# Kernel tuning notes

Measured on AMD Instinct MI355X. Metric: run time of the kernel, lower is better.

Reference implementation:

```python
import jax, jax.numpy as jnp
import numpy as np

B, F, NP, DIM, H, DH = 4, 16, 196, 512, 8, 64  # batch, frames, patches, dim, heads, dim_head
N = 1 + F * NP  # sequence length incl CLS


def setup_inputs() -> dict:
    key = jax.random.key(0)
    k1, k2, k3, k4 = jax.random.split(key, 4)
    return {
        "x": jax.random.normal(k1, (B, N, DIM), dtype=jnp.float32),
        "W_qkv": jax.random.normal(k2, (DIM, 3 * H * DH), dtype=jnp.float32) * 0.05,
        "W_out": jax.random.normal(k3, (H * DH, DIM), dtype=jnp.float32) * 0.05,
        "b_out": jax.random.normal(k4, (DIM,), dtype=jnp.float32) * 0.05,
        "f": F,
    }


def _attn(q, k, v):
    # q: [bb, i, d], k/v: [bb, j, d]
    sim = jnp.einsum('bid,bjd->bij', q, k)
    a = jax.nn.softmax(sim, axis=-1)
    return jnp.einsum('bij,bjd->bid', a, v)


def reference(x, W_qkv, W_out, b_out, f):
    b, n_tot, dim = x.shape
    h, d = H, DH
    scale = d ** (-0.5)
    qkv = x @ W_qkv  # [b, N, 3*h*d]
    q, k, v = jnp.split(qkv, 3, axis=-1)

    def to_bh(t):  # b n (h d) -> (b h) n d
        return t.reshape(b, n_tot, h, d).transpose(0, 2, 1, 3).reshape(b * h, n_tot, d)

    q, k, v = map(to_bh, (q, k, v))
    q = q * scale

    cls_q, q_ = q[:, :1], q[:, 1:]
    cls_k, k_ = k[:, :1], k[:, 1:]
    cls_v, v_ = v[:, :1], v[:, 1:]

    # CLS token attends over the full sequence
    cls_out = _attn(cls_q, k, v)  # [(b h), 1, d]

    # spatial factorization: (b h) (f n) d -> (b h f) n d
    n = (n_tot - 1) // f
    def split_f(t):
        return t.reshape(b * h * f, n, d)
    q_, k_, v_ = map(split_f, (q_, k_, v_))

    # repeat CLS k/v per frame: b () d -> (b r) () d with r = f
    cls_k_r = jnp.repeat(cls_k, f, axis=0)
    cls_v_r = jnp.repeat(cls_v, f, axis=0)
    k_ = jnp.concatenate([cls_k_r, k_], axis=1)  # [(b h f), n+1, d]
    v_ = jnp.concatenate([cls_v_r, v_], axis=1)

    out = _attn(q_, k_, v_)  # [(b h f), n, d]
    out = out.reshape(b * h, f * n, d)
    out = jnp.concatenate([cls_out, out], axis=1)  # [(b h), N, d]
    out = out.reshape(b, h, n_tot, d).transpose(0, 2, 1, 3).reshape(b, n_tot, h * d)
    return out @ W_out + b_out
```

## Files before the change

kernel.cpp:

```cpp
#include <hip/hip_runtime.h>
#include <math.h>

#define B_   4
#define F_   16
#define NP_  196
#define DIM_ 512
#define H_   8
#define DH_  64
#define NTOT 3137
#define BH_  32
#define MROWS 12548
#define QSZ_ ((size_t)BH_ * NTOT * DH_)
#define KVPAD 224
#define PSTRIDE 232
#define NCHUNK 13

typedef unsigned short u16;
typedef __attribute__((ext_vector_type(8))) short    bf16x8;
typedef __attribute__((ext_vector_type(8))) unsigned short u16x8;
typedef __attribute__((ext_vector_type(4))) unsigned short u16x4;
typedef __attribute__((ext_vector_type(4))) float    f32x4;

__device__ __forceinline__ u16 f2bf(float f) {
    unsigned int u = __float_as_uint(f);
    unsigned int r = (u + 0x7FFFu + ((u >> 16) & 1u)) >> 16;
    return (u16)r;
}
__device__ __forceinline__ float bf2f(u16 u) {
    return __uint_as_float(((unsigned int)u) << 16);
}

__device__ __forceinline__ void gl2lds16(const u16* g, u16* l) {
    __builtin_amdgcn_global_load_lds(
        (const __attribute__((address_space(1))) unsigned int*)(g),
        (__attribute__((address_space(3))) unsigned int*)(l),
        16, 0, 0);
}

__global__ __launch_bounds__(256) void convert_x_kernel(
    const float* __restrict__ x, u16* __restrict__ xbf)
{
    int idx = blockIdx.x * 256 + threadIdx.x;
    float4 v = ((const float4*)x)[idx];
    u16x4 p = { f2bf(v.x), f2bf(v.y), f2bf(v.z), f2bf(v.w) };
    *(u16x4*)(&xbf[(size_t)idx * 4]) = p;
}

__global__ __launch_bounds__(256) void transpose_bf16_kernel(
    const float* __restrict__ src, u16* __restrict__ dst, int R, int C)
{
    __shared__ float t[32][33];
    const int tx = threadIdx.x & 31, ty = threadIdx.x >> 5;
    const int c0 = blockIdx.x * 32, r0 = blockIdx.y * 32;
    #pragma unroll
    for (int i = 0; i < 4; ++i) {
        int r = ty + i * 8;
        t[r][tx] = src[(size_t)(r0 + r) * C + c0 + tx];
    }
    __syncthreads();
    #pragma unroll
    for (int i = 0; i < 4; ++i) {
        int cc = ty + i * 8;
        dst[(size_t)(c0 + cc) * R + r0 + tx] = f2bf(t[tx][cc]);
    }
}

template<int MODE, int MI>
__global__ __launch_bounds__(256, 2) void gemm_bf16_mfma(
    const u16* __restrict__ A, const u16* __restrict__ BT,
    u16* __restrict__ Cq, u16* __restrict__ Ck, u16* __restrict__ Cv,
    float* __restrict__ Cout, const float* __restrict__ bias)
{
    constexpr int ASUB = MI * 2;
    __shared__ alignas(16) u16 Asm[2][ASUB * 512];
    __shared__ alignas(16) u16 Bsm[2][8 * 512];

    const int tid  = threadIdx.x;
    const int wave = tid >> 6, lane = tid & 63;
    const int wr = wave >> 1, wc = wave & 1;
    const int lm = lane & 15, lq = lane >> 4;
    const int row0 = blockIdx.y * (MI * 32);
    const int col0 = blockIdx.x * 128;

    f32x4 acc[MI][4];
    #pragma unroll
    for (int i = 0; i < MI; ++i)
        #pragma unroll
        for (int j = 0; j < 4; ++j) acc[i][j] = (f32x4){0.f, 0.f, 0.f, 0.f};

    auto stage = [&](int k0, int buf) {
        #pragma unroll
        for (int i = 0; i < ASUB / 4; ++i) {
            int s = wave * (ASUB / 4) + i;
            int arow = row0 + s * 16 + lm;
            if (arow >= MROWS) arow = MROWS - 1;
            gl2lds16(A + (size_t)arow * 512 + k0 + lq * 8, &Asm[buf][s * 512 + lane * 8]);
        }
        #pragma unroll
        for (int i = 0; i < 2; ++i) {
            int s = wave * 2 + i;
            int brow = col0 + s * 16 + lm;
            gl2lds16(BT + (size_t)brow * 512 + k0 + lq * 8, &Bsm[buf][s * 512 + lane * 8]);
        }
    };

    stage(0, 0);
    for (int it = 0; it < 16; ++it) {
        __syncthreads();
        if (it < 15) stage((it + 1) * 32, (it + 1) & 1);
        const int buf = it & 1;
        bf16x8 af[MI], bf[4];
        #pragma unroll
        for (int mi = 0; mi < MI; ++mi)
            af[mi] = *(const bf16x8*)(&Asm[buf][(wr * MI + mi) * 512 + lane * 8]);
        #pragma unroll
        for (int ni = 0; ni < 4; ++ni)
            bf[ni] = *(const bf16x8*)(&Bsm[buf][(wc * 4 + ni) * 512 + lane * 8]);
        #pragma unroll
        for (int mi = 0; mi < MI; ++mi)
            #pragma unroll
            for (int ni = 0; ni < 4; ++ni)
                acc[mi][ni] = __builtin_amdgcn_mfma_f32_16x16x32_bf16(
                    af[mi], bf[ni], acc[mi][ni], 0, 0, 0);
    }

    if (MODE == 0) {
        const int t3 = col0 >> 9;
        #pragma unroll
        for (int mi = 0; mi < MI; ++mi) {
            #pragma unroll
            for (int r = 0; r < 4; ++r) {
                int gr = row0 + wr * (MI * 16) + mi * 16 + lq * 4 + r;
                if (gr >= MROWS) continue;
                int b = gr / NTOT;
                int n = gr - b * NTOT;
                #pragma unroll
                for (int ni = 0; ni < 4; ++ni) {
                    int gc = col0 + wc * 64 + ni * 16 + lm;
                    int rem = gc & 511;
                    int h = rem >> 6, d = rem & 63;
                    size_t tok = (size_t)(b * H_ + h) * NTOT + n;
                    float v = acc[mi][ni][r];
                    if (t3 == 0)      Cq[tok * 64 + d] = f2bf(v * 0.125f);
                    else if (t3 == 1) Ck[tok * 64 + d] = f2bf(v);
                    else              Cv[tok * 64 + d] = f2bf(v);
                }
            }
        }
    } else {
        float bb[4];
        #pragma unroll
        for (int ni = 0; ni < 4; ++ni)
            bb[ni] = bias[col0 + wc * 64 + ni * 16 + lm];
        #pragma unroll
        for (int mi = 0; mi < MI; ++mi) {
            #pragma unroll
            for (int r = 0; r < 4; ++r) {
                int gr = row0 + wr * (MI * 16) + mi * 16 + lq * 4 + r;
                if (gr >= MROWS) continue;
                #pragma unroll
                for (int ni = 0; ni < 4; ++ni) {
                    int gc = col0 + wc * 64 + ni * 16 + lm;
                    Cout[(size_t)gr * 512 + gc] = acc[mi][ni][r] + bb[ni];
                }
            }
        }
    }
}

__global__ __launch_bounds__(256) void vt_build_kernel(
    const u16* __restrict__ vb, u16* __restrict__ vT)
{
    const int g = blockIdx.x;
    const int bh = g >> 4, f = g & 15;
    const int d = threadIdx.x & 63, jq = threadIdx.x >> 6;
    const int j0 = blockIdx.y * 32;
    u16* dst = vT + ((size_t)g * 64 + d) * KVPAD;
    #pragma unroll
    for (int i = 0; i < 8; ++i) {
        int jj = j0 + i * 4 + jq;
        u16 val = 0;
        if (jj <= 196) {
            int n = (jj == 0) ? 0 : (1 + f * NP_ + jj - 1);
            val = vb[((size_t)bh * NTOT + n) * 64 + d];
        }
        dst[jj] = val;
    }
}

__global__ __launch_bounds__(256) void attn_mfma_kernel(
    const u16* __restrict__ qb, const u16* __restrict__ kb,
    const u16* __restrict__ vT, u16* __restrict__ attn)
{
    __shared__ alignas(16) u16 Pbuf[4 * 16 * PSTRIDE];

    const int tid  = threadIdx.x;
    const int wave = tid >> 6, lane = tid & 63;
    const int lm = lane & 15, lq = lane >> 4;
    const int task = blockIdx.x * 4 + wave;
    const int mt = task % 13;
    const int gf = task / 13;
    const int f  = gf & 15;
    const int bh = gf >> 4;

    const int rq = min(mt * 16 + lm, 195);
    const u16* qrow = qb + ((size_t)bh * NTOT + (1 + f * NP_ + rq)) * 64;
    bf16x8 qf0 = *(const bf16x8*)(qrow + lq * 8);
    bf16x8 qf1 = *(const bf16x8*)(qrow + 32 + lq * 8);

    f32x4 S[13];
    #pragma unroll
    for (int nt = 0; nt < 13; ++nt) {
        int rkc = min(nt * 16 + lm, 196);
        int nk = (rkc == 0) ? 0 : (1 + f * NP_ + rkc - 1);
        const u16* krow = kb + ((size_t)bh * NTOT + nk) * 64;
        bf16x8 kf0 = *(const bf16x8*)(krow + lq * 8);
        bf16x8 kf1 = *(const bf16x8*)(krow + 32 + lq * 8);
        f32x4 z = (f32x4){0.f, 0.f, 0.f, 0.f};
        z = __builtin_amdgcn_mfma_f32_16x16x32_bf16(qf0, kf0, z, 0, 0, 0);
        z = __builtin_amdgcn_mfma_f32_16x16x32_bf16(qf1, kf1, z, 0, 0, 0);
        S[nt] = z;
    }

    #pragma unroll
    for (int nt = 0; nt < 13; ++nt)
        if (nt * 16 + lm >= 197) {
            S[nt][0] = -INFINITY; S[nt][1] = -INFINITY;
            S[nt][2] = -INFINITY; S[nt][3] = -INFINITY;
        }

    float invl[4];
    #pragma unroll
    for (int r = 0; r < 4; ++r) {
        float mx = -INFINITY;
        #pragma unroll
        for (int nt = 0; nt < 13; ++nt) mx = fmaxf(mx, S[nt][r]);
        mx = fmaxf(mx, __shfl_xor(mx, 1, 64));
        mx = fmaxf(mx, __shfl_xor(mx, 2, 64));
        mx = fmaxf(mx, __shfl_xor(mx, 4, 64));
        mx = fmaxf(mx, __shfl_xor(mx, 8, 64));
        float sum = 0.f;
        #pragma unroll
        for (int nt = 0; nt < 13; ++nt) {
            float p = __expf(S[nt][r] - mx);
            S[nt][r] = p;
            sum += p;
        }
        sum += __shfl_xor(sum, 1, 64);
        sum += __shfl_xor(sum, 2, 64);
        sum += __shfl_xor(sum, 4, 64);
        sum += __shfl_xor(sum, 8, 64);
        invl[r] = 1.f / sum;
    }

    u16* P = Pbuf + wave * 16 * PSTRIDE;
    #pragma unroll
    for (int nt = 0; nt < 13; ++nt) {
        int col = nt * 16 + lm;
        #pragma unroll
        for (int r = 0; r < 4; ++r)
            P[(lq * 4 + r) * PSTRIDE + col] = f2bf(S[nt][r]);
    }
    {
        u16x4 z4 = {0, 0, 0, 0};
        *(u16x4*)(P + lm * PSTRIDE + 208 + lq * 4) = z4;
    }

    f32x4 O[4];
    #pragma unroll
    for (int nd = 0; nd < 4; ++nd) O[nd] = (f32x4){0.f, 0.f, 0.f, 0.f};
    const u16* vbase = vT + (size_t)(bh * 16 + f) * 64 * KVPAD;
    #pragma unroll
    for (int ks = 0; ks < 7; ++ks) {
        bf16x8 pf = *(const bf16x8*)(P + lm * PSTRIDE + ks * 32 + lq * 8);
        #pragma unroll
        for (int nd = 0; nd < 4; ++nd) {
            bf16x8 vf = *(const bf16x8*)(vbase + (size_t)(nd * 16 + lm) * KVPAD + ks * 32 + lq * 8);
            O[nd] = __builtin_amdgcn_mfma_f32_16x16x32_bf16(pf, vf, O[nd], 0, 0, 0);
        }
    }

    const int b = bh >> 3, h = bh & 7;
    #pragma unroll
    for (int r = 0; r < 4; ++r) {
        int rql = mt * 16 + lq * 4 + r;
        if (rql >= 196) continue;
        int n = 1 + f * NP_ + rql;
        u16* dst = attn + ((size_t)b * NTOT + n) * 512 + h * 64;
        float s = invl[r];
        #pragma unroll
        for (int nd = 0; nd < 4; ++nd)
            dst[nd * 16 + lm] = f2bf(O[nd][r] * s);
    }
}

__global__ __launch_bounds__(256) void attn_cls_partial_kernel(
    const u16* __restrict__ qb, const u16* __restrict__ kb,
    const u16* __restrict__ vb, float* __restrict__ cls_m,
    float* __restrict__ cls_l, float* __restrict__ cls_o)
{
    __shared__ float qs[64];
    __shared__ float redm[4], redl[4];
    __shared__ float ps[256];
    __shared__ float so[4][64];

    const int c = blockIdx.x, bh = blockIdx.y;
    const int t = threadIdx.x;
    const int lane = t & 63, w = t >> 6;

    if (t < 64) qs[t] = bf2f(qb[(size_t)bh * NTOT * 64 + t]);
    __syncthreads();

    const int j = c * 256 + t;
    const bool valid = (j < NTOT);
    const int jc = valid ? j : (NTOT - 1);
    const u16* krow = kb + ((size_t)bh * NTOT + jc) * 64;
    float s0 = 0.f, s1 = 0.f, s2 = 0.f, s3 = 0.f;
    #pragma unroll
    for (int i = 0; i < 8; ++i) {
        u16x8 k8 = *(const u16x8*)(krow + i * 8);
        const float* qp = qs + i * 8;
        s0 = fmaf(qp[0], bf2f(k8[0]), s0);
        s1 = fmaf(qp[1], bf2f(k8[1]), s1);
        s2 = fmaf(qp[2], bf2f(k8[2]), s2);
        s3 = fmaf(qp[3], bf2f(k8[3]), s3);
        s0 = fmaf(qp[4], bf2f(k8[4]), s0);
        s1 = fmaf(qp[5], bf2f(k8[5]), s1);
        s2 = fmaf(qp[6], bf2f(k8[6]), s2);
        s3 = fmaf(qp[7], bf2f(k8[7]), s3);
    }
    float s = (s0 + s1) + (s2 + s3);
    if (!valid) s = -INFINITY;

    float mx = s;
    #pragma unroll
    for (int off = 1; off < 64; off <<= 1) mx = fmaxf(mx, __shfl_xor(mx, off, 64));
    if (lane == 0) redm[w] = mx;
    __syncthreads();
    mx = fmaxf(fmaxf(redm[0], redm[1]), fmaxf(redm[2], redm[3]));

    float pv = __expf(s - mx);
    float l = pv;
    #pragma unroll
    for (int off = 1; off < 64; off <<= 1) l += __shfl_xor(l, off, 64);
    if (lane == 0) redl[w] = l;
    ps[t] = pv;
    __syncthreads();
    l = redl[0] + redl[1] + redl[2] + redl[3];

    const int d = lane, part = w;
    float o = 0.f;
    #pragma unroll 8
    for (int i = 0; i < 64; ++i) {
        int jj = c * 256 + part * 64 + i;
        int jjc = (jj < NTOT) ? jj : (NTOT - 1);
        o = fmaf(ps[part * 64 + i], bf2f(vb[((size_t)bh * NTOT + jjc) * 64 + d]), o);
    }
    so[part][d] = o;
    __syncthreads();
    if (t < 64) {
        float O = so[0][t] + so[1][t] + so[2][t] + so[3][t];
        int pi = bh * NCHUNK + c;
        cls_o[(size_t)pi * 64 + t] = O;
        if (t == 0) { cls_m[pi] = mx; cls_l[pi] = l; }
    }
}

__global__ __launch_bounds__(64) void attn_cls_merge_kernel(
    const float* __restrict__ cls_m, const float* __restrict__ cls_l,
    const float* __restrict__ cls_o, u16* __restrict__ attn)
{
    const int bh = blockIdx.x, lane = threadIdx.x;
    float M = -INFINITY;
    #pragma unroll
    for (int p = 0; p < NCHUNK; ++p) M = fmaxf(M, cls_m[bh * NCHUNK + p]);
    float L = 0.f, O = 0.f;
    #pragma unroll
    for (int p = 0; p < NCHUNK; ++p) {
        float al = __expf(cls_m[bh * NCHUNK + p] - M);
        L += cls_l[bh * NCHUNK + p] * al;
        O += cls_o[(size_t)(bh * NCHUNK + p) * 64 + lane] * al;
    }
    const int b = bh >> 3, h = bh & 7;
    attn[(size_t)b * NTOT * 512 + h * 64 + lane] = f2bf(O / L);
}

extern "C" void kernel_launch(void* const* d_in, const int* in_sizes, int n_in,
                              void* d_out, int out_size, void* d_ws, size_t ws_size,
                              hipStream_t stream) {
    const float* x    = (const float*)d_in[0];
    const float* wqkv = (const float*)d_in[1];
    const float* wout = (const float*)d_in[2];
    const float* bout = (const float*)d_in[3];

    u16* p = (u16*)d_ws;
    u16* xbf   = p;                    p += (size_t)MROWS * 512;
    u16* attn  = xbf;
    u16* wqkvT = p;                    p += (size_t)1536 * 512;
    u16* woutT = p;                    p += (size_t)512 * 512;
    u16* qbuf  = p;                    p += QSZ_;
    u16* kbuf  = p;                    p += QSZ_;
    u16* vbuf  = p;                    p += QSZ_;
    u16* vT    = p;                    p += (size_t)BH_ * 16 * 64 * KVPAD;
    float* clsws = (float*)p;
    float* cls_m = clsws;
    float* cls_l = clsws + BH_ * NCHUNK;
    float* cls_o = clsws + 2 * BH_ * NCHUNK;
    float* outp  = (float*)d_out;

    convert_x_kernel<<<6274, 256, 0, stream>>>(x, xbf);
    transpose_bf16_kernel<<<dim3(48, 16), 256, 0, stream>>>(wqkv, wqkvT, 512, 1536);
    transpose_bf16_kernel<<<dim3(16, 16), 256, 0, stream>>>(wout, woutT, 512, 512);
    gemm_bf16_mfma<0, 8><<<dim3(12, 50), 256, 0, stream>>>(
        xbf, wqkvT, qbuf, kbuf, vbuf, nullptr, nullptr);
    vt_build_kernel<<<dim3(512, 7), 256, 0, stream>>>(vbuf, vT);
    attn_mfma_kernel<<<1664, 256, 0, stream>>>(qbuf, kbuf, vT, attn);
    attn_cls_partial_kernel<<<dim3(NCHUNK, 32), 256, 0, stream>>>(
        qbuf, kbuf, vbuf, cls_m, cls_l, cls_o);
    attn_cls_merge_kernel<<<32, 64, 0, stream>>>(cls_m, cls_l, cls_o, attn);
    gemm_bf16_mfma<1, 4><<<dim3(4, 99), 256, 0, stream>>>(
        attn, woutT, nullptr, nullptr, nullptr, outp, bout);
}
```

Measured before the change: 268.7 us.

## Restructure GEMM to keep full-K B tile in LDS and stream A from global

The bf16 MFMA GEMM now loads the entire 64-column by 512-K slice of the transposed weight into LDS once per block, then has each wave read its A rows directly from global memory into registers, with no per-K-step staging or barriers. The old version double-buffered both A and B in LDS. Tiles become 256 rows by 64 columns, so the grids change, and the QKV epilogue hoists the head, destination buffer and scale out of the inner loop. This removes the LDS round-trip and the synchronisation for A. In exchange, A loads are uncoalesced-ish direct global reads, B uses 64KB of LDS, and occupancy may drop.

```diff
diff --git a/kernel.cpp b/kernel.cpp
--- a/kernel.cpp
+++ b/kernel.cpp
@@ -65,104 +65,93 @@
     }
 }
 
-template<int MODE, int MI>
-__global__ __launch_bounds__(256, 2) void gemm_bf16_mfma(
+template<int MODE>
+__global__ __launch_bounds__(256) void gemm_bf16_mfma(
     const u16* __restrict__ A, const u16* __restrict__ BT,
     u16* __restrict__ Cq, u16* __restrict__ Ck, u16* __restrict__ Cv,
     float* __restrict__ Cout, const float* __restrict__ bias)
 {
-    constexpr int ASUB = MI * 2;
-    __shared__ alignas(16) u16 Asm[2][ASUB * 512];
-    __shared__ alignas(16) u16 Bsm[2][8 * 512];
+    __shared__ alignas(16) u16 Bs[64 * 512];
 
     const int tid  = threadIdx.x;
     const int wave = tid >> 6, lane = tid & 63;
-    const int wr = wave >> 1, wc = wave & 1;
     const int lm = lane & 15, lq = lane >> 4;
-    const int row0 = blockIdx.y * (MI * 32);
-    const int col0 = blockIdx.x * 128;
-
-    f32x4 acc[MI][4];
-    #pragma unroll
-    for (int i = 0; i < MI; ++i)
+    const int col0 = blockIdx.x * 64;
+    const int rows0 = blockIdx.y * 256;
+
+    #pragma unroll
+    for (int i = 0; i < 16; ++i) {
+        int sub = wave * 16 + i;
+        int s = sub >> 2, n = sub & 3;
+        gl2lds16(BT + (size_t)(col0 + n * 16 + lm) * 512 + s * 32 + lq * 8,
+                 &Bs[sub * 512 + lane * 8]);
+    }
+    __syncthreads();
+
+    const int rbase = rows0 + wave * 64;
+    const u16* aptr[4];
+    #pragma unroll
+    for (int ri = 0; ri < 4; ++ri) {
+        int r = rbase + ri * 16 + lm;
+        if (r >= MROWS) r = MROWS - 1;
+        aptr[ri] = A + (size_t)r * 512 + lq * 8;
+    }
+
+    f32x4 acc[4][4];
+    #pragma unroll
+    for (int i = 0; i < 4; ++i)
         #pragma unroll
         for (int j = 0; j < 4; ++j) acc[i][j] = (f32x4){0.f, 0.f, 0.f, 0.f};
 
-    auto stage = [&](int k0, int buf) {
-        #pragma unroll
-        for (int i = 0; i < ASUB / 4; ++i) {
-            int s = wave * (ASUB / 4) + i;
-            int arow = row0 + s * 16 + lm;
-            if (arow >= MROWS) arow = MROWS - 1;
-            gl2lds16(A + (size_t)arow * 512 + k0 + lq * 8, &Asm[buf][s * 512 + lane * 8]);
-        }
-        #pragma unroll
-        for (int i = 0; i < 2; ++i) {
-            int s = wave * 2 + i;
-            int brow = col0 + s * 16 + lm;
-            gl2lds16(BT + (size_t)brow * 512 + k0 + lq * 8, &Bsm[buf][s * 512 + lane * 8]);
-        }
-    };
-
-    stage(0, 0);
-    for (int it = 0; it < 16; ++it) {
-        __syncthreads();
-        if (it < 15) stage((it + 1) * 32, (it + 1) & 1);
-        const int buf = it & 1;
-        bf16x8 af[MI], bf[4];
-        #pragma unroll
-        for (int mi = 0; mi < MI; ++mi)
-            af[mi] = *(const bf16x8*)(&Asm[buf][(wr * MI + mi) * 512 + lane * 8]);
+    #pragma unroll 4
+    for (int s = 0; s < 16; ++s) {
+        bf16x8 bfr[4];
         #pragma unroll
         for (int ni = 0; ni < 4; ++ni)
-            bf[ni] = *(const bf16x8*)(&Bsm[buf][(wc * 4 + ni) * 512 + lane * 8]);
-        #pragma unroll
-        for (int mi = 0; mi < MI; ++mi)
+            bfr[ni] = *(const bf16x8*)(&Bs[(s * 4 + ni) * 512 + lane * 8]);
+        #pragma unroll
+        for (int ri = 0; ri < 4; ++ri) {
+            bf16x8 af = *(const bf16x8*)(aptr[ri] + s * 32);
             #pragma unroll
             for (int ni = 0; ni < 4; ++ni)
-                acc[mi][ni] = __builtin_amdgcn_mfma_f32_16x16x32_bf16(
-                    af[mi], bf[ni], acc[mi][ni], 0, 0, 0);
+                acc[ri][ni] = __builtin_amdgcn_mfma_f32_16x16x32_bf16(
+                    af, bfr[ni], acc[ri][ni], 0, 0, 0);
+        }
     }
 
     if (MODE == 0) {
         const int t3 = col0 >> 9;
-        #pragma unroll
-        for (int mi = 0; mi < MI; ++mi) {
+        const int h  = (col0 >> 6) & 7;
+        u16* dst3 = (t3 == 0) ? Cq : (t3 == 1) ? Ck : Cv;
+        const float scale = (t3 == 0) ? 0.125f : 1.0f;
+        #pragma unroll
+        for (int ri = 0; ri < 4; ++ri) {
             #pragma unroll
             for (int r = 0; r < 4; ++r) {
-                int gr = row0 + wr * (MI * 16) + mi * 16 + lq * 4 + r;
+                int gr = rbase + ri * 16 + lq * 4 + r;
                 if (gr >= MROWS) continue;
                 int b = gr / NTOT;
                 int n = gr - b * NTOT;
+                size_t tok = (size_t)(b * H_ + h) * NTOT + n;
                 #pragma unroll
-                for (int ni = 0; ni < 4; ++ni) {
-                    int gc = col0 + wc * 64 + ni * 16 + lm;
-                    int rem = gc & 511;
-                    int h = rem >> 6, d = rem & 63;
-                    size_t tok = (size_t)(b * H_ + h) * NTOT + n;
-                    float v = acc[mi][ni][r];
-                    if (t3 == 0)      Cq[tok * 64 + d] = f2bf(v * 0.125f);
-                    else if (t3 == 1) Ck[tok * 64 + d] = f2bf(v);
-                    else              Cv[tok * 64 + d] = f2bf(v);
-                }
+                for (int ni = 0; ni < 4; ++ni)
+                    dst3[tok * 64 + ni * 16 + lm] = f2bf(acc[ri][ni][r] * scale);
             }
         }
     } else {
         float bb[4];
         #pragma unroll
         for (int ni = 0; ni < 4; ++ni)
-            bb[ni] = bias[col0 + wc * 64 + ni * 16 + lm];
-        #pragma unroll
-        for (int mi = 0; mi < MI; ++mi) {
+            bb[ni] = bias[col0 + ni * 16 + lm];
+        #pragma unroll
+        for (int ri = 0; ri < 4; ++ri) {
             #pragma unroll
             for (int r = 0; r < 4; ++r) {
-                int gr = row0 + wr * (MI * 16) + mi * 16 + lq * 4 + r;
+                int gr = rbase + ri * 16 + lq * 4 + r;
                 if (gr >= MROWS) continue;
                 #pragma unroll
-                for (int ni = 0; ni < 4; ++ni) {
-                    int gc = col0 + wc * 64 + ni * 16 + lm;
-                    Cout[(size_t)gr * 512 + gc] = acc[mi][ni][r] + bb[ni];
-                }
+                for (int ni = 0; ni < 4; ++ni)
+                    Cout[(size_t)gr * 512 + col0 + ni * 16 + lm] = acc[ri][ni][r] + bb[ni];
             }
         }
     }
@@ -411,13 +400,13 @@
     convert_x_kernel<<<6274, 256, 0, stream>>>(x, xbf);
     transpose_bf16_kernel<<<dim3(48, 16), 256, 0, stream>>>(wqkv, wqkvT, 512, 1536);
     transpose_bf16_kernel<<<dim3(16, 16), 256, 0, stream>>>(wout, woutT, 512, 512);
-    gemm_bf16_mfma<0, 8><<<dim3(12, 50), 256, 0, stream>>>(
+    gemm_bf16_mfma<0><<<dim3(24, 50), 256, 0, stream>>>(
         xbf, wqkvT, qbuf, kbuf, vbuf, nullptr, nullptr);
     vt_build_kernel<<<dim3(512, 7), 256, 0, stream>>>(vbuf, vT);
     attn_mfma_kernel<<<1664, 256, 0, stream>>>(qbuf, kbuf, vT, attn);
     attn_cls_partial_kernel<<<dim3(NCHUNK, 32), 256, 0, stream>>>(
         qbuf, kbuf, vbuf, cls_m, cls_l, cls_o);
     attn_cls_merge_kernel<<<32, 64, 0, stream>>>(cls_m, cls_l, cls_o, attn);
-    gemm_bf16_mfma<1, 4><<<dim3(4, 99), 256, 0, stream>>>(
+    gemm_bf16_mfma<1><<<dim3(8, 50), 256, 0, stream>>>(
         attn, woutT, nullptr, nullptr, nullptr, outp, bout);
 }
```

Result: faster. 258.4 us (-3.9%).
